# Kernel optimization log

Measured on AMD Instinct MI355X. Metric: run time of the kernel, lower is better.

## Reference

```python
import jax, jax.numpy as jnp
import numpy as np

D_MODEL = 1024
NUM_HEAD = 16
D_HEAD = 64


def setup_inputs() -> dict:
    key = jax.random.key(0)
    ks = jax.random.split(key, 9)
    b, p = 8, 1024
    s = 1.0 / np.sqrt(D_MODEL)
    inp = {
        "x": jax.random.normal(ks[0], (b, p, D_MODEL), jnp.float32),
        "w_q": jax.random.uniform(ks[1], (D_MODEL, D_MODEL), jnp.float32, -s, s),
        "b_q": jax.random.uniform(ks[2], (D_MODEL,), jnp.float32, -s, s),
        "w_k": jax.random.uniform(ks[3], (D_MODEL, D_MODEL), jnp.float32, -s, s),
        "b_k": jax.random.uniform(ks[4], (D_MODEL,), jnp.float32, -s, s),
        "w_v": jax.random.uniform(ks[5], (D_MODEL, D_MODEL), jnp.float32, -s, s),
        "b_v": jax.random.uniform(ks[6], (D_MODEL,), jnp.float32, -s, s),
        "w_o": jax.random.uniform(ks[7], (D_MODEL, D_MODEL), jnp.float32, -s, s),
        "b_o": jax.random.uniform(ks[8], (D_MODEL,), jnp.float32, -s, s),
    }
    return inp


def reference(x, w_q, b_q, w_k, b_k, w_v, b_v, w_o, b_o):
    b, p, _ = x.shape
    # projections (torch Linear: y = x @ W.T + b; here weights stored [in,out])
    q = x @ w_q + b_q
    k = x @ w_k + b_k
    v = x @ w_v + b_v
    # [b, h, p, d]
    q = q.reshape(b, p, NUM_HEAD, D_HEAD).transpose(0, 2, 1, 3)
    k = k.reshape(b, p, NUM_HEAD, D_HEAD).transpose(0, 2, 1, 3)
    v = v.reshape(b, p, NUM_HEAD, D_HEAD).transpose(0, 2, 1, 3)
    scale = 1.0 / np.sqrt(D_HEAD).astype(np.float32)
    scores = jnp.einsum("bhqd,bhkd->bhqk", q, k) * scale
    attn = jax.nn.softmax(scores, axis=-1)
    out = jnp.einsum("bhqk,bhkd->bhqd", attn, v)
    out = out.transpose(0, 2, 1, 3).reshape(b, p, D_MODEL)
    return out @ w_o + b_o
```

## Files before the change

kernel.cpp:

```cpp
#include <hip/hip_runtime.h>
#include <stdint.h>


typedef __attribute__((ext_vector_type(8))) short short8;
typedef __attribute__((ext_vector_type(4))) short s16x4;
typedef __attribute__((ext_vector_type(4))) float f32x4;

__device__ __forceinline__ short f2bf(float f) {
  unsigned u = __builtin_bit_cast(unsigned, f);
  u += 0x7fffu + ((u >> 16) & 1u);
  return (short)(u >> 16);
}

__device__ __forceinline__ unsigned pk2bf(float a, float b) {
  unsigned ua = __builtin_bit_cast(unsigned, a);
  unsigned ub = __builtin_bit_cast(unsigned, b);
  ua += 0x7fffu + ((ua >> 16) & 1u);
  ub += 0x7fffu + ((ub >> 16) & 1u);
  return (ua >> 16) | (ub & 0xffff0000u);
}

typedef __attribute__((address_space(3))) void lds_void;
typedef __attribute__((address_space(1))) void gbl_void;
#define GLD16(gp, lp) \
  __builtin_amdgcn_global_load_lds((gbl_void*)(gp), (lds_void*)(lp), 16, 0, 0)

#define MFMA(a, b, c) __builtin_amdgcn_mfma_f32_16x16x32_bf16((a), (b), (c), 0, 0, 0)

__global__ __launch_bounds__(256) void k_prep(const float* __restrict__ x,
                                              short* __restrict__ xb,
                                              const float* __restrict__ s0,
                                              const float* __restrict__ s1,
                                              const float* __restrict__ s2,
                                              const float* __restrict__ s3,
                                              short* __restrict__ d0,
                                              short* __restrict__ d1,
                                              short* __restrict__ d2,
                                              short* __restrict__ d3) {
  if (blockIdx.z == 4) {
    int t = threadIdx.y * 32 + threadIdx.x;
    int bid = blockIdx.y * 32 + blockIdx.x;
#pragma unroll
    for (int j = 0; j < 4; ++j) {
      int i = (bid * 1024 + j * 256 + t) * 8;
      const float4* s = (const float4*)(x + i);
      float4 f0 = s[0], f1 = s[1];
      short8 o;
      o[0] = f2bf(f0.x); o[1] = f2bf(f0.y); o[2] = f2bf(f0.z); o[3] = f2bf(f0.w);
      o[4] = f2bf(f1.x); o[5] = f2bf(f1.y); o[6] = f2bf(f1.z); o[7] = f2bf(f1.w);
      *(short8*)(xb + i) = o;
    }
    return;
  }
  __shared__ float tile[32][33];
  const float* srcs[4] = {s0, s1, s2, s3};
  short* dsts[4] = {d0, d1, d2, d3};
  const float* src = srcs[blockIdx.z];
  short* dst = dsts[blockIdx.z];
  int tx = threadIdx.x, ty = threadIdx.y;
  int x0 = blockIdx.x * 32, y0 = blockIdx.y * 32;
#pragma unroll
  for (int i = 0; i < 32; i += 8)
    tile[ty + i][tx] = src[(y0 + ty + i) * 1024 + x0 + tx];
  __syncthreads();
#pragma unroll
  for (int i = 0; i < 32; i += 8)
    dst[(x0 + ty + i) * 1024 + y0 + tx] = f2bf(tile[tx][ty + i]);
}

template <int MODE>
__global__ __launch_bounds__(256, 3) void k_gemm(const short* __restrict__ A,
                                                 const short* __restrict__ Bt,
                                                 const float* __restrict__ bias0,
                                                 const float* __restrict__ bias1,
                                                 const float* __restrict__ bias2,
                                                 short* __restrict__ o0,
                                                 short* __restrict__ o1,
                                                 short* __restrict__ o2,
                                                 float* __restrict__ of) {
  __shared__ __align__(16) short a_lds[128 * 64];
  __shared__ __align__(16) short b_lds[128 * 64];
  const int tid = threadIdx.x;
  const int l = blockIdx.x;
  const int m0 = ((((l & 7) << 3) | ((l >> 3) & 7))) << 7;
  const int n0 = (l >> 6) << 7;
  const int w = tid >> 6;
  const int lane = tid & 63;
  const int ll = lane & 15;
  const int qd = lane >> 4;
  const int wm = (w & 1) * 64;
  const int wn = (w >> 1) * 64;

  const int srow = tid >> 3;
  const int schunk = ((tid & 7) ^ (srow & 7)) * 8;
  const short* ag = A + (long)(m0 + srow) * 1024 + schunk;
  const short* bg = Bt + (long)(n0 + srow) * 1024 + schunk;

  f32x4 acc[4][4] = {};

  for (int kt = 0; kt < 1024; kt += 64) {
#pragma unroll
    for (int j = 0; j < 4; ++j) {
      GLD16(ag + j * 32768 + kt, &a_lds[j * 2048 + tid * 8]);
      GLD16(bg + j * 32768 + kt, &b_lds[j * 2048 + tid * 8]);
    }
    __syncthreads();
#pragma unroll
    for (int kh = 0; kh < 2; ++kh) {
      const int xoff = (((kh * 4 + qd) ^ (ll & 7)) * 8);
      short8 af[4], bfr[4];
#pragma unroll
      for (int mt = 0; mt < 4; ++mt)
        af[mt] = *(const short8*)&a_lds[(wm + mt * 16 + ll) * 64 + xoff];
#pragma unroll
      for (int nt = 0; nt < 4; ++nt)
        bfr[nt] = *(const short8*)&b_lds[(wn + nt * 16 + ll) * 64 + xoff];
#pragma unroll
      for (int mt = 0; mt < 4; ++mt)
#pragma unroll
        for (int nt = 0; nt < 4; ++nt)
          acc[mt][nt] = MFMA(af[mt], bfr[nt], acc[mt][nt]);
    }
    __syncthreads();
  }

  if (MODE == 0) {
#pragma unroll
    for (int nt = 0; nt < 4; ++nt) {
      int n = n0 + wn + nt * 16 + ll;
      int which = n >> 10;
      int nl = n & 1023;
      int h = nl >> 6, d = n & 63;
      if (which == 2) {
        float bv = bias2[nl];
        const int b = m0 >> 10;
        const int p0 = (m0 & 1023) + wm;
#pragma unroll
        for (int mt = 0; mt < 4; ++mt) {
          int p = p0 + mt * 16 + qd * 4;
          int2 pk;
          pk.x = (int)pk2bf(acc[mt][nt][0] + bv, acc[mt][nt][1] + bv);
          pk.y = (int)pk2bf(acc[mt][nt][2] + bv, acc[mt][nt][3] + bv);
          *(int2*)&o2[(long)(b * 16 + h) * 65536 + d * 1024 + p] = pk;
        }
      } else {
        float bv = (which == 0) ? bias0[nl] : bias1[nl];
        float sc = (which == 0) ? 0.125f : 1.0f;
        short* o = (which == 0) ? o0 : o1;
#pragma unroll
        for (int mt = 0; mt < 4; ++mt) {
#pragma unroll
          for (int r = 0; r < 4; ++r) {
            int m = m0 + wm + mt * 16 + qd * 4 + r;
            int b = m >> 10, p = m & 1023;
            o[(long)(b * 16 + h) * 65536 + p * 64 + d] = f2bf((acc[mt][nt][r] + bv) * sc);
          }
        }
      }
    }
  } else {
#pragma unroll
    for (int nt = 0; nt < 4; ++nt) {
      int n = n0 + wn + nt * 16 + ll;
      float bv = bias0[n];
#pragma unroll
      for (int mt = 0; mt < 4; ++mt) {
#pragma unroll
        for (int r = 0; r < 4; ++r) {
          int m = m0 + wm + mt * 16 + qd * 4 + r;
          of[(long)m * 1024 + n] = acc[mt][nt][r] + bv;
        }
      }
    }
  }
}

__global__ __launch_bounds__(256, 4) void k_attn(const short* __restrict__ Q,
                                                 const short* __restrict__ K,
                                                 const short* __restrict__ VT,
                                                 short* __restrict__ O) {
  __shared__ __align__(16) short k_lds[4096];
  __shared__ __align__(16) short vt_lds[4096];
  __shared__ __align__(16) short p_lds[4][32 * 72];
  const int tid = threadIdx.x;
  const int w = tid >> 6, lane = tid & 63, ll = lane & 15, qd = lane >> 4;
  const int bh = blockIdx.y, qb = blockIdx.x;
  const long hoff = (long)bh * 65536;
  const int qr0 = qb * 128 + w * 32;

  const short* qg = Q + hoff + (long)(qr0 + ll) * 64 + qd * 8;
  short8 qf[2][2];
  qf[0][0] = *(const short8*)qg;
  qf[0][1] = *(const short8*)(qg + 32);
  qf[1][0] = *(const short8*)(qg + 1024);
  qf[1][1] = *(const short8*)(qg + 1024 + 32);

  const int sr = tid >> 3;
  const int swz = (tid & 7) ^ (sr & 7);
  const short* kg = K + hoff + sr * 64 + swz * 8;
  const short* vg = VT + hoff + (long)sr * 1024 + swz * 8;
  short* kl0 = &k_lds[tid * 8];
  short* kl1 = &k_lds[2048 + tid * 8];
  short* vl0 = &vt_lds[tid * 8];
  short* vl1 = &vt_lds[2048 + tid * 8];

  const int swzr = ll & 7;
  const int fro0 = ll * 64 + ((qd ^ swzr) * 8);
  const int fro1 = ll * 64 + (((4 + qd) ^ swzr) * 8);
  short* pw = &p_lds[w][0];

  f32x4 oacc[2][4] = {};
  float l_part[2] = {0.f, 0.f};

  for (int c = 0; c < 16; ++c) {
    GLD16(kg + c * 4096, kl0);
    GLD16(kg + c * 4096 + 2048, kl1);
    GLD16(vg + c * 64, vl0);
    GLD16(vg + c * 64 + 32768, vl1);
    __syncthreads();

    f32x4 s[2][4];
#pragma unroll
    for (int jt = 0; jt < 4; ++jt) {
      short8 kf0 = *(const short8*)&k_lds[jt * 1024 + fro0];
      short8 kf1 = *(const short8*)&k_lds[jt * 1024 + fro1];
      f32x4 t0 = {};
      t0 = MFMA(kf0, qf[0][0], t0);
      t0 = MFMA(kf1, qf[0][1], t0);
      s[0][jt] = t0;
      f32x4 t1 = {};
      t1 = MFMA(kf0, qf[1][0], t1);
      t1 = MFMA(kf1, qf[1][1], t1);
      s[1][jt] = t1;
    }

    short8 pf[2][2];
#pragma unroll
    for (int g = 0; g < 2; ++g) {
      float rs = 0.f;
#pragma unroll
      for (int jt = 0; jt < 4; ++jt)
#pragma unroll
        for (int r = 0; r < 4; ++r) {
          float e = __expf(s[g][jt][r]);
          s[g][jt][r] = e;
          rs += e;
        }
      l_part[g] += rs;
      short* pg = pw + (g * 16 + ll) * 72;
#pragma unroll
      for (int jt = 0; jt < 4; ++jt) {
        int2 pk;
        pk.x = (int)pk2bf(s[g][jt][0], s[g][jt][1]);
        pk.y = (int)pk2bf(s[g][jt][2], s[g][jt][3]);
        *(int2*)&pg[jt * 16 + qd * 4] = pk;
      }
      pf[g][0] = *(const short8*)&pg[qd * 8];
      pf[g][1] = *(const short8*)&pg[32 + qd * 8];
    }

#pragma unroll
    for (int dt = 0; dt < 4; ++dt) {
      short8 vf0 = *(const short8*)&vt_lds[dt * 1024 + fro0];
      short8 vf1 = *(const short8*)&vt_lds[dt * 1024 + fro1];
      oacc[0][dt] = MFMA(vf0, pf[0][0], oacc[0][dt]);
      oacc[0][dt] = MFMA(vf1, pf[0][1], oacc[0][dt]);
      oacc[1][dt] = MFMA(vf0, pf[1][0], oacc[1][dt]);
      oacc[1][dt] = MFMA(vf1, pf[1][1], oacc[1][dt]);
    }
    __syncthreads();
  }

  const int b = bh >> 4, h = bh & 15;
#pragma unroll
  for (int g = 0; g < 2; ++g) {
    float l = l_part[g];
    l += __shfl_xor(l, 16, 64);
    l += __shfl_xor(l, 32, 64);
    const float inv = 1.0f / l;
    const long row = (long)(b * 1024 + qr0 + g * 16 + ll);
#pragma unroll
    for (int dt = 0; dt < 4; ++dt) {
      int2 ov;
      ov.x = (int)pk2bf(oacc[g][dt][0] * inv, oacc[g][dt][1] * inv);
      ov.y = (int)pk2bf(oacc[g][dt][2] * inv, oacc[g][dt][3] * inv);
      *(int2*)&O[row * 1024 + h * 64 + dt * 16 + qd * 4] = ov;
    }
  }
}

extern "C" void kernel_launch(void* const* d_in, const int* in_sizes, int n_in,
                              void* d_out, int out_size, void* d_ws, size_t ws_size,
                              hipStream_t stream) {
  const float* x   = (const float*)d_in[0];
  const float* w_q = (const float*)d_in[1];
  const float* b_q = (const float*)d_in[2];
  const float* w_k = (const float*)d_in[3];
  const float* b_k = (const float*)d_in[4];
  const float* w_v = (const float*)d_in[5];
  const float* b_v = (const float*)d_in[6];
  const float* w_o = (const float*)d_in[7];
  const float* b_o = (const float*)d_in[8];

  char* ws = (char*)d_ws;
  short* xb    = (short*)(ws);
  short* wqkvT = (short*)(ws + (16ull << 20));
  short* woT   = (short*)(ws + (22ull << 20));
  short* qw    = (short*)(ws + (24ull << 20));
  short* kw    = (short*)(ws + (40ull << 20));
  short* vw    = (short*)(ws + (56ull << 20));

  k_prep<<<dim3(32, 32, 5), dim3(32, 8), 0, stream>>>(
      x, xb, w_q, w_k, w_v, w_o,
      wqkvT, wqkvT + (1 << 20), wqkvT + (2 << 20), woT);

  k_gemm<0><<<1536, 256, 0, stream>>>(xb, wqkvT, b_q, b_k, b_v,
                                      qw, kw, vw, nullptr);

  k_attn<<<dim3(8, 128), 256, 0, stream>>>(qw, kw, vw, xb);

  k_gemm<1><<<512, 256, 0, stream>>>(xb, woT, b_o, nullptr, nullptr,
                                     nullptr, nullptr, nullptr, (float*)d_out);
}
```

Measured before the change: 244.3 us.

## Double-buffer attention K/V tiles, keep P in registers, use exp2 and hardware bf16 packing

The attention kernel now double-buffers K and V^T tiles in LDS, prefetching the next chunk while computing the current one. K rows are permuted at load time so the score MFMA output layout matches the PV operand layout, which removes the P round-trip through LDS. It also folds log2(e) into the Q scale so softmax can use v_exp_f32 directly, swaps manual bf16 rounding for v_cvt_pk_bf16_f32, adds s_setprio around MFMA blocks, and remaps the 1D grid so heads are grouped per XCD for L2 locality. The risks are correctness of the row permutation and extra LDS usage that may reduce occupancy.

```diff
diff --git a/kernel.cpp b/kernel.cpp
--- a/kernel.cpp
+++ b/kernel.cpp
@@ -18,6 +18,18 @@
   ua += 0x7fffu + ((ua >> 16) & 1u);
   ub += 0x7fffu + ((ub >> 16) & 1u);
   return (ua >> 16) | (ub & 0xffff0000u);
+}
+
+__device__ __forceinline__ unsigned cvtpk(float a, float b) {
+  unsigned r;
+  asm("v_cvt_pk_bf16_f32 %0, %1, %2" : "=v"(r) : "v"(a), "v"(b));
+  return r;
+}
+
+__device__ __forceinline__ float fexp2(float x) {
+  float r;
+  asm("v_exp_f32 %0, %1" : "=v"(r) : "v"(x));
+  return r;
 }
 
 typedef __attribute__((address_space(3))) void lds_void;
@@ -145,7 +157,7 @@
         }
       } else {
         float bv = (which == 0) ? bias0[nl] : bias1[nl];
-        float sc = (which == 0) ? 0.125f : 1.0f;
+        float sc = (which == 0) ? 0.18033688f : 1.0f;
         short* o = (which == 0) ? o0 : o1;
 #pragma unroll
         for (int mt = 0; mt < 4; ++mt) {
@@ -179,12 +191,15 @@
                                                  const short* __restrict__ K,
                                                  const short* __restrict__ VT,
                                                  short* __restrict__ O) {
-  __shared__ __align__(16) short k_lds[4096];
-  __shared__ __align__(16) short vt_lds[4096];
-  __shared__ __align__(16) short p_lds[4][32 * 72];
+  __shared__ __align__(16) short k_lds[2][4096];
+  __shared__ __align__(16) short vt_lds[2][4096];
   const int tid = threadIdx.x;
   const int w = tid >> 6, lane = tid & 63, ll = lane & 15, qd = lane >> 4;
-  const int bh = blockIdx.y, qb = blockIdx.x;
+  const int bid = blockIdx.x;
+  const int xcd = bid & 7;
+  const int inner = bid >> 3;
+  const int bh = xcd * 16 + (inner & 15);
+  const int qb = inner >> 4;
   const long hoff = (long)bh * 65536;
   const int qr0 = qb * 128 + w * 32;
 
@@ -197,33 +212,39 @@
 
   const int sr = tid >> 3;
   const int swz = (tid & 7) ^ (sr & 7);
-  const short* kg = K + hoff + sr * 64 + swz * 8;
+  const int pr = (sr & 0x23) | ((sr & 0x0C) << 1) | ((sr & 0x10) >> 2);
+  const short* kg = K + hoff + pr * 64 + swz * 8;
   const short* vg = VT + hoff + (long)sr * 1024 + swz * 8;
-  short* kl0 = &k_lds[tid * 8];
-  short* kl1 = &k_lds[2048 + tid * 8];
-  short* vl0 = &vt_lds[tid * 8];
-  short* vl1 = &vt_lds[2048 + tid * 8];
 
   const int swzr = ll & 7;
   const int fro0 = ll * 64 + ((qd ^ swzr) * 8);
   const int fro1 = ll * 64 + (((4 + qd) ^ swzr) * 8);
-  short* pw = &p_lds[w][0];
 
   f32x4 oacc[2][4] = {};
   float l_part[2] = {0.f, 0.f};
 
+  GLD16(kg, &k_lds[0][tid * 8]);
+  GLD16(kg + 2048, &k_lds[0][2048 + tid * 8]);
+  GLD16(vg, &vt_lds[0][tid * 8]);
+  GLD16(vg + 32768, &vt_lds[0][2048 + tid * 8]);
+  __syncthreads();
+
+#pragma unroll 2
   for (int c = 0; c < 16; ++c) {
-    GLD16(kg + c * 4096, kl0);
-    GLD16(kg + c * 4096 + 2048, kl1);
-    GLD16(vg + c * 64, vl0);
-    GLD16(vg + c * 64 + 32768, vl1);
-    __syncthreads();
+    const int cur = c & 1, nxt = cur ^ 1;
+    if (c < 15) {
+      GLD16(kg + (c + 1) * 4096, &k_lds[nxt][tid * 8]);
+      GLD16(kg + (c + 1) * 4096 + 2048, &k_lds[nxt][2048 + tid * 8]);
+      GLD16(vg + (c + 1) * 64, &vt_lds[nxt][tid * 8]);
+      GLD16(vg + (c + 1) * 64 + 32768, &vt_lds[nxt][2048 + tid * 8]);
+    }
 
     f32x4 s[2][4];
+    __builtin_amdgcn_s_setprio(1);
 #pragma unroll
     for (int jt = 0; jt < 4; ++jt) {
-      short8 kf0 = *(const short8*)&k_lds[jt * 1024 + fro0];
-      short8 kf1 = *(const short8*)&k_lds[jt * 1024 + fro1];
+      short8 kf0 = *(const short8*)&k_lds[cur][jt * 1024 + fro0];
+      short8 kf1 = *(const short8*)&k_lds[cur][jt * 1024 + fro1];
       f32x4 t0 = {};
       t0 = MFMA(kf0, qf[0][0], t0);
       t0 = MFMA(kf1, qf[0][1], t0);
@@ -233,6 +254,7 @@
       t1 = MFMA(kf1, qf[1][1], t1);
       s[1][jt] = t1;
     }
+    __builtin_amdgcn_s_setprio(0);
 
     short8 pf[2][2];
 #pragma unroll
@@ -242,32 +264,33 @@
       for (int jt = 0; jt < 4; ++jt)
 #pragma unroll
         for (int r = 0; r < 4; ++r) {
-          float e = __expf(s[g][jt][r]);
+          float e = fexp2(s[g][jt][r]);
           s[g][jt][r] = e;
           rs += e;
         }
       l_part[g] += rs;
-      short* pg = pw + (g * 16 + ll) * 72;
-#pragma unroll
-      for (int jt = 0; jt < 4; ++jt) {
-        int2 pk;
-        pk.x = (int)pk2bf(s[g][jt][0], s[g][jt][1]);
-        pk.y = (int)pk2bf(s[g][jt][2], s[g][jt][3]);
-        *(int2*)&pg[jt * 16 + qd * 4] = pk;
+#pragma unroll
+      for (int u = 0; u < 2; ++u) {
+        union { short8 v; unsigned x[4]; } pk;
+        pk.x[0] = cvtpk(s[g][2 * u][0], s[g][2 * u][1]);
+        pk.x[1] = cvtpk(s[g][2 * u][2], s[g][2 * u][3]);
+        pk.x[2] = cvtpk(s[g][2 * u + 1][0], s[g][2 * u + 1][1]);
+        pk.x[3] = cvtpk(s[g][2 * u + 1][2], s[g][2 * u + 1][3]);
+        pf[g][u] = pk.v;
       }
-      pf[g][0] = *(const short8*)&pg[qd * 8];
-      pf[g][1] = *(const short8*)&pg[32 + qd * 8];
-    }
-
+    }
+
+    __builtin_amdgcn_s_setprio(1);
 #pragma unroll
     for (int dt = 0; dt < 4; ++dt) {
-      short8 vf0 = *(const short8*)&vt_lds[dt * 1024 + fro0];
-      short8 vf1 = *(const short8*)&vt_lds[dt * 1024 + fro1];
+      short8 vf0 = *(const short8*)&vt_lds[cur][dt * 1024 + fro0];
+      short8 vf1 = *(const short8*)&vt_lds[cur][dt * 1024 + fro1];
       oacc[0][dt] = MFMA(vf0, pf[0][0], oacc[0][dt]);
       oacc[0][dt] = MFMA(vf1, pf[0][1], oacc[0][dt]);
       oacc[1][dt] = MFMA(vf0, pf[1][0], oacc[1][dt]);
       oacc[1][dt] = MFMA(vf1, pf[1][1], oacc[1][dt]);
     }
+    __builtin_amdgcn_s_setprio(0);
     __syncthreads();
   }
 
@@ -282,8 +305,8 @@
 #pragma unroll
     for (int dt = 0; dt < 4; ++dt) {
       int2 ov;
-      ov.x = (int)pk2bf(oacc[g][dt][0] * inv, oacc[g][dt][1] * inv);
-      ov.y = (int)pk2bf(oacc[g][dt][2] * inv, oacc[g][dt][3] * inv);
+      ov.x = (int)cvtpk(oacc[g][dt][0] * inv, oacc[g][dt][1] * inv);
+      ov.y = (int)cvtpk(oacc[g][dt][2] * inv, oacc[g][dt][3] * inv);
       *(int2*)&O[row * 1024 + h * 64 + dt * 16 + qd * 4] = ov;
     }
   }
@@ -317,7 +340,7 @@
   k_gemm<0><<<1536, 256, 0, stream>>>(xb, wqkvT, b_q, b_k, b_v,
                                       qw, kw, vw, nullptr);
 
-  k_attn<<<dim3(8, 128), 256, 0, stream>>>(qw, kw, vw, xb);
+  k_attn<<<dim3(1024), 256, 0, stream>>>(qw, kw, vw, xb);
 
   k_gemm<1><<<512, 256, 0, stream>>>(xb, woT, b_o, nullptr, nullptr,
                                      nullptr, nullptr, nullptr, (float*)d_out);
```

After: 231.9 us. 5.1% less time.
